# Kernel optimization log

Hardware: AMD Instinct MI355X
Metric: run time of the kernel (lower is better)

## Reference

```python
import jax, jax.numpy as jnp
import numpy as np

N, E, R = 100000, 600000, 2      # nodes, edges per relation, relations
IN, H, DH = 128, 8, 16           # input dim, heads, per-head hidden
D = H * DH                       # 128 = hidden_dim * n_heads
RIN, RH = 64, 16                 # relation input / hidden dims
SLOPE = 0.2                      # leaky relu negative slope


def _leaky(v):
    return jnp.where(v >= 0, v, SLOPE * v)


def setup_inputs() -> dict:
    key = jax.random.key(0)
    ks = jax.random.split(key, 18)
    nrm = lambda k, shape, s: jax.random.normal(k, shape, jnp.float32) * s
    sc = 1.0 / np.sqrt(D).astype(np.float32)
    return {
        'x': nrm(ks[0], (N, IN), 1.0),
        'src': jax.random.randint(ks[1], (R, E), 0, N, jnp.int32),
        'dst': jax.random.randint(ks[2], (R, E), 0, N, jnp.int32),
        'rel_emb': nrm(ks[3], (R, RIN), 1.0),
        'Wp': nrm(ks[4], (IN, D), sc), 'bp': jnp.zeros((D,), jnp.float32),
        'Wn': nrm(ks[5], (D, D), sc), 'bn': jnp.zeros((D,), jnp.float32),
        'Wsrc': nrm(ks[6], (R, D, D), sc), 'bsrc': jnp.zeros((R, D), jnp.float32),
        'Wrel': nrm(ks[7], (R, RIN, H * 2 * DH), 1.0 / np.sqrt(RIN).astype(np.float32)),
        'resW': nrm(ks[8], (IN, D), sc), 'resb': jnp.zeros((D,), jnp.float32),
        'res_alpha': nrm(ks[9], (1,), 1.0),
        'crossW': nrm(ks[10], (R, H, DH), 1.0 / np.sqrt(DH).astype(np.float32)),
        'Wprop': nrm(ks[11], (R, RIN, H * RH), 1.0 / np.sqrt(RIN).astype(np.float32)),
        'bprop': jnp.zeros((R, H * RH), jnp.float32),
    }


def reference(x, src, dst, rel_emb, Wp, bp, Wn, bn, Wsrc, bsrc, Wrel,
              resW, resb, res_alpha, crossW, Wprop, bprop):
    # projection_layer (R_HGT) then node_transformation_layers (layer input transform)
    xp = x @ Wp + bp                                  # [N, D]
    h = (xp @ Wn + bn).reshape(N, H, DH)              # [N, H, DH] dst-side features
    res = (xp @ resW + resb).reshape(N, H, DH)        # res_fc(input_dst)

    def per_rel(sr, dr, e_emb, Ws, bs, Wr):
        # relation_src_node_transformation + relation-conditioned attention
        s = (h.reshape(N, D) @ Ws + bs).reshape(N, H, DH)   # src messages
        a = (e_emb @ Wr).reshape(H, 2, DH)                  # relation attn vectors
        sc_src = (s * a[:, 0]).sum(-1)                      # [N, H]
        sc_dst = (h * a[:, 1]).sum(-1)                      # [N, H]
        e_sc = _leaky(sc_src[sr] + sc_dst[dr])              # [E, H]
        # edge softmax over incoming edges of each dst node
        m = jax.lax.stop_gradient(jax.ops.segment_max(e_sc, dr, num_segments=N))
        ex = jnp.exp(e_sc - m[dr])
        den = jax.ops.segment_sum(ex, dr, num_segments=N)
        alpha = ex / den[dr]                                # [E, H]
        msg = alpha[:, :, None] * s[sr]                     # [E, H, DH]
        return jax.ops.segment_sum(msg, dr, num_segments=N)  # [N, H, DH]

    out = jax.vmap(per_rel)(src, dst, rel_emb, Wsrc, bsrc, Wrel)  # [R, N, H, DH]

    # sigmoid-gated residual (shared per dst ntype)
    g = jax.nn.sigmoid(res_alpha)[0]
    out = out * g + res[None] * (1.0 - g)

    # RelationCrossing: attention across the R relation-specific dst features
    def cross(cw):
        attn = jax.nn.softmax(_leaky((out * cw[None, None]).sum(-1)), axis=0)  # [R,N,H]
        return (attn[..., None] * out).sum(0)                                  # [N,H,DH]

    fused = jax.vmap(cross)(crossW).reshape(R, N, D)      # [R, N, D]

    # relation_propagation_layer
    rel_out = jnp.einsum('ri,rio->ro', rel_emb, Wprop) + bprop  # [R, H*RH]
    return fused, rel_out
```

## Files before the change

kernel.cpp:

```cpp
#include <hip/hip_runtime.h>
#include <math.h>

#define NN 100000
#define EE 600000
#define RR 2
#define DD 128
#define HH 8
#define DHH 16
#define RN (RR * NN)
#define NT 26
#define MTOT 6250
#define CHUNK 4096
#define NCH ((EE + CHUNK - 1) / CHUNK)
#define BINW 512
#define NBIN ((NN + BINW - 1) / BINW)
#define BCAPD 4096

typedef unsigned short ushort_t;
typedef short bf16x8 __attribute__((ext_vector_type(8)));
typedef float f32x4 __attribute__((ext_vector_type(4)));

__device__ __forceinline__ float lrelu(float v) { return v >= 0.f ? v : 0.2f * v; }

__device__ __forceinline__ ushort_t f2bf(float f) {
    unsigned int u = __float_as_uint(f);
    u = (u + 0x7FFFu + ((u >> 16) & 1u)) >> 16;
    return (ushort_t)u;
}
__device__ __forceinline__ float bf2f(ushort_t u) {
    return __uint_as_float(((unsigned int)u) << 16);
}

__global__ void k_prep(const float* __restrict__ rel_emb, const float* __restrict__ Wrel,
                       const float* __restrict__ Wprop, const float* __restrict__ bprop,
                       float* __restrict__ avec, float* __restrict__ rel_out) {
    int tid = threadIdx.x;
    for (int idx = tid; idx < RR * 256; idx += 256) {
        int r = idx >> 8, o = idx & 255;
        float acc = 0.f;
        for (int i = 0; i < 64; ++i)
            acc += rel_emb[r * 64 + i] * Wrel[(r * 64 + i) * 256 + o];
        avec[idx] = acc;
    }
    {
        int r = tid >> 7, o = tid & 127;
        float acc = bprop[tid];
        for (int i = 0; i < 64; ++i)
            acc += rel_emb[r * 64 + i] * Wprop[(r * 64 + i) * 128 + o];
        rel_out[tid] = acc;
    }
}

__global__ __launch_bounds__(128) void k_compose1(
    const float* __restrict__ Wp, const float* __restrict__ bp,
    const float* __restrict__ Wn, const float* __restrict__ bn,
    const float* __restrict__ resW, const float* __restrict__ resb,
    float* __restrict__ Wpn, float* __restrict__ bpn,
    float* __restrict__ Wres_c, float* __restrict__ bres_c) {
    __shared__ float row[DD];
    const int rrow = blockIdx.x, tid = threadIdx.x;
    row[tid] = Wp[rrow * DD + tid];
    __syncthreads();
    float acc1 = 0.f, acc2 = 0.f;
    for (int k = 0; k < DD; ++k) {
        float wv = row[k];
        acc1 = fmaf(wv, Wn[k * DD + tid], acc1);
        acc2 = fmaf(wv, resW[k * DD + tid], acc2);
    }
    Wpn[rrow * DD + tid] = acc1;
    Wres_c[rrow * DD + tid] = acc2;
    if (rrow == 0) {
        float b1 = 0.f, b2 = 0.f;
        for (int k = 0; k < DD; ++k) {
            b1 = fmaf(bp[k], Wn[k * DD + tid], b1);
            b2 = fmaf(bp[k], resW[k * DD + tid], b2);
        }
        bpn[tid] = b1 + bn[tid];
        bres_c[tid] = b2 + resb[tid];
    }
}

__global__ __launch_bounds__(128) void k_compose2(
    const float* __restrict__ Wpn, const float* __restrict__ bpn,
    const float* __restrict__ Wsrc, const float* __restrict__ bsrc,
    const float* __restrict__ avec,
    float* __restrict__ Ws_c, float* __restrict__ bs_c,
    float* __restrict__ VdstT, float* __restrict__ cdst) {
    __shared__ float row[DD];
    const int rel = blockIdx.x, rrow = blockIdx.y, tid = threadIdx.x;
    row[tid] = Wpn[rrow * DD + tid];
    __syncthreads();
    const float* W = Wsrc + (size_t)rel * DD * DD;
    float acc = 0.f;
    for (int k = 0; k < DD; ++k) acc = fmaf(row[k], W[k * DD + tid], acc);
    Ws_c[(size_t)rel * DD * DD + rrow * DD + tid] = acc;
    if (tid < HH) {
        float v = 0.f;
        for (int d = 0; d < 16; ++d)
            v += row[tid * 16 + d] * avec[rel * 256 + tid * 32 + 16 + d];
        VdstT[(rel * HH + tid) * DD + rrow] = v;
    }
    if (rrow == 0) {
        float b = 0.f;
        for (int k = 0; k < DD; ++k) b = fmaf(bpn[k], W[k * DD + tid], b);
        bs_c[rel * DD + tid] = b + bsrc[rel * DD + tid];
        if (rel == 0 && tid < 16) {
            int r2 = tid >> 3, h2 = tid & 7;
            float c2 = 0.f;
            for (int d = 0; d < 16; ++d)
                c2 += bpn[h2 * 16 + d] * avec[r2 * 256 + h2 * 32 + 16 + d];
            cdst[tid] = c2;
        }
    }
}

__global__ __launch_bounds__(256) void k_pack(
    const float* __restrict__ Ws_c, const float* __restrict__ Wres_c,
    const float* __restrict__ VdstT, const float* __restrict__ avec,
    const float* __restrict__ bs_c, short* __restrict__ Wpk,
    float* __restrict__ csrc) {
    const int t = blockIdx.x;
    const int kt = threadIdx.x >> 6;
    const int l = threadIdx.x & 63;
    const int c16 = l & 15;
    bf16x8 v;
    #pragma unroll
    for (int j = 0; j < 8; ++j) {
        int k = kt * 32 + (l >> 4) * 8 + j;
        float f;
        if (t < 24) {
            int m = t >> 3;
            int col = (t & 7) * 16 + c16;
            const float* W = (m == 0) ? Ws_c : (m == 1) ? Ws_c + DD * DD : Wres_c;
            f = W[k * DD + col];
        } else if (t == 24) {
            f = VdstT[c16 * DD + k];
        } else {
            int rel = c16 >> 3, h = c16 & 7;
            f = 0.f;
            for (int d = 0; d < 16; ++d)
                f += Ws_c[(size_t)rel * DD * DD + k * DD + h * 16 + d]
                     * avec[rel * 256 + h * 32 + d];
        }
        v[j] = (short)f2bf(f);
    }
    *(bf16x8*)(Wpk + ((size_t)(t * 4 + kt) * 64 + l) * 8) = v;
    if (t == 25 && threadIdx.x < 16) {
        int rel = threadIdx.x >> 3, h = threadIdx.x & 7;
        float c = 0.f;
        for (int d = 0; d < 16; ++d)
            c += bs_c[rel * DD + h * 16 + d] * avec[rel * 256 + h * 32 + d];
        csrc[threadIdx.x] = c;
    }
}

__global__ __launch_bounds__(256) void k_node3(
    const float* __restrict__ x, const short* __restrict__ Wpk,
    const float* __restrict__ bs_c, const float* __restrict__ bres_c,
    const float* __restrict__ cdst, const float* __restrict__ csrc,
    ushort_t* __restrict__ s_out, ushort_t* __restrict__ res_out,
    float* __restrict__ sc_src, float* __restrict__ sc_dst) {
    const int tid = threadIdx.x;
    const int l = tid & 63;
    const int w = tid >> 6;
    const int m16 = l & 15, g4 = l >> 4;
    const int mt = blockIdx.x * 4 + w;
    const bool live = (mt < MTOT);
    const int nb = (live ? mt : MTOT - 1) * 16;

    bf16x8 af[4];
    const float* xrow = x + (size_t)(nb + m16) * DD + g4 * 8;
    #pragma unroll
    for (int kt = 0; kt < 4; ++kt) {
        float4 v0 = *(const float4*)(xrow + kt * 32);
        float4 v1 = *(const float4*)(xrow + kt * 32 + 4);
        af[kt][0] = (short)f2bf(v0.x); af[kt][1] = (short)f2bf(v0.y);
        af[kt][2] = (short)f2bf(v0.z); af[kt][3] = (short)f2bf(v0.w);
        af[kt][4] = (short)f2bf(v1.x); af[kt][5] = (short)f2bf(v1.y);
        af[kt][6] = (short)f2bf(v1.z); af[kt][7] = (short)f2bf(v1.w);
    }

    for (int t = 0; t < NT; ++t) {
        f32x4 acc = {0.f, 0.f, 0.f, 0.f};
        #pragma unroll
        for (int kt = 0; kt < 4; ++kt) {
            bf16x8 b = *(const bf16x8*)(Wpk + ((size_t)(t * 4 + kt) * 64 + l) * 8);
            acc = __builtin_amdgcn_mfma_f32_16x16x32_bf16(af[kt], b, acc, 0, 0, 0);
        }
        if (!live) continue;
        if (t < 16) {
            const int rel = t >> 3, head = t & 7;
            const float bb = bs_c[rel * DD + head * 16 + m16];
            #pragma unroll
            for (int r = 0; r < 4; ++r) {
                const int node = nb + g4 * 4 + r;
                s_out[((size_t)rel * NN + node) * DD + head * 16 + m16] =
                    f2bf(acc[r] + bb);
            }
        } else if (t < 24) {
            const int col = (t - 16) * 16 + m16;
            const float bb = bres_c[col];
            #pragma unroll
            for (int r = 0; r < 4; ++r) {
                const int node = nb + g4 * 4 + r;
                res_out[(size_t)node * DD + col] = f2bf(acc[r] + bb);
            }
        } else if (t == 24) {
            const int rel = m16 >> 3, head = m16 & 7;
            const float bb = cdst[m16];
            #pragma unroll
            for (int r = 0; r < 4; ++r) {
                const int node = nb + g4 * 4 + r;
                sc_dst[((size_t)rel * NN + node) * HH + head] = acc[r] + bb;
            }
        } else {
            const int rel = m16 >> 3, head = m16 & 7;
            const float bb = csrc[m16];
            #pragma unroll
            for (int r = 0; r < 4; ++r) {
                const int node = nb + g4 * 4 + r;
                sc_src[((size_t)rel * NN + node) * HH + head] = acc[r] + bb;
            }
        }
    }
}

__global__ __launch_bounds__(256) void k_binct(const int* __restrict__ dst,
                                               int* __restrict__ binct) {
    __shared__ int bins[NBIN];
    const int blk = blockIdx.x, rel = blockIdx.y, tid = threadIdx.x;
    if (tid < NBIN) bins[tid] = 0;
    __syncthreads();
    for (int i = tid; i < CHUNK; i += 256) {
        int e = blk * CHUNK + i;
        if (e < EE) atomicAdd(&bins[dst[rel * EE + e] >> 9], 1);
    }
    __syncthreads();
    if (tid < NBIN) binct[((rel * NCH) + blk) * NBIN + tid] = bins[tid];
}

__global__ __launch_bounds__(512) void k_binscan(const int* __restrict__ binct,
                                                 int* __restrict__ runoff,
                                                 int* __restrict__ binstart,
                                                 int* __restrict__ row_ptr) {
    __shared__ int tot[512];
    const int t = threadIdx.x;
    int run = 0;
    if (t < RR * NBIN) {
        const int rel = t / NBIN, bin = t - rel * NBIN;
        for (int blk = 0; blk < NCH; ++blk) {
            int idx = ((rel * NCH) + blk) * NBIN + bin;
            int v = binct[idx];
            runoff[idx] = run;
            run += v;
        }
    }
    tot[t] = (t < RR * NBIN) ? run : 0;
    __syncthreads();
    for (int off = 1; off < 512; off <<= 1) {
        int v = (t >= off) ? tot[t - off] : 0;
        __syncthreads();
        tot[t] += v;
        __syncthreads();
    }
    if (t < RR * NBIN) binstart[t] = tot[t] - run;
    if (t == 0) {
        binstart[RR * NBIN] = RR * EE;
        row_ptr[RN] = RR * EE;
    }
}

__global__ __launch_bounds__(256) void k_binfill(
    const int* __restrict__ src, const int* __restrict__ dst,
    const int* __restrict__ runoff, const int* __restrict__ binstart,
    int* __restrict__ ebuf) {
    __shared__ int ofs[NBIN];
    __shared__ int bins[NBIN];
    const int blk = blockIdx.x, rel = blockIdx.y, tid = threadIdx.x;
    if (tid < NBIN) {
        ofs[tid] = binstart[rel * NBIN + tid] + runoff[((rel * NCH) + blk) * NBIN + tid];
        bins[tid] = 0;
    }
    __syncthreads();
    for (int i = tid; i < CHUNK; i += 256) {
        int e = blk * CHUNK + i;
        if (e < EE) {
            int d = dst[rel * EE + e];
            int b = d >> 9;
            int loc = atomicAdd(&bins[b], 1);
            ebuf[ofs[b] + loc] = ((d & 511) << 17) | src[rel * EE + e];
        }
    }
}

__global__ __launch_bounds__(256) void k_binfin(
    const int* __restrict__ ebuf, const int* __restrict__ binstart,
    int* __restrict__ row_ptr, int* __restrict__ esrc) {
    __shared__ int keys[BCAPD];
    __shared__ int cnt[BINW];
    __shared__ int scn[BINW];
    __shared__ int part[256];
    const int bin = blockIdx.x, rel = blockIdx.y, tid = threadIdx.x;
    const int p0 = binstart[rel * NBIN + bin];
    const int p1 = binstart[rel * NBIN + bin + 1];
    const int cntE = p1 - p0;
    const bool inlds = (cntE <= BCAPD);
    const int n0 = bin * BINW;
    const int nw = min(BINW, NN - n0);

    cnt[2 * tid] = 0; cnt[2 * tid + 1] = 0;
    __syncthreads();
    for (int i = tid; i < cntE; i += 256) {
        int k = ebuf[p0 + i];
        if (inlds) keys[i] = k;
        atomicAdd(&cnt[k >> 17], 1);
    }
    __syncthreads();
    int a = cnt[2 * tid], b = cnt[2 * tid + 1];
    part[tid] = a + b;
    __syncthreads();
    for (int off = 1; off < 256; off <<= 1) {
        int v = (tid >= off) ? part[tid - off] : 0;
        __syncthreads();
        part[tid] += v;
        __syncthreads();
    }
    int excl = (tid == 0) ? 0 : part[tid - 1];
    scn[2 * tid] = excl;
    scn[2 * tid + 1] = excl + a;
    cnt[2 * tid] = 0; cnt[2 * tid + 1] = 0;
    __syncthreads();
    for (int n = tid; n < nw; n += 256)
        row_ptr[rel * NN + n0 + n] = p0 + scn[n];
    for (int i = tid; i < cntE; i += 256) {
        int k = inlds ? keys[i] : ebuf[p0 + i];
        int low = k >> 17;
        int slot = atomicAdd(&cnt[low], 1);
        esrc[p0 + scn[low] + slot] = k & 0x1FFFF;
    }
}

__global__ __launch_bounds__(256) void k_gather_cross(
    const int* __restrict__ esrc, const int* __restrict__ row_ptr,
    const float* __restrict__ sc_src, const float* __restrict__ sc_dst,
    const ushort_t* __restrict__ s, const ushort_t* __restrict__ res_buf,
    const float* __restrict__ res_alpha, const float* __restrict__ crossW,
    float* __restrict__ out) {
    int n = blockIdx.x * 4 + (threadIdx.x >> 6);
    if (n >= NN) return;
    const int lane = threadIdx.x & 63;
    const int g = lane >> 5;
    const int j = lane & 31;
    const int h = j >> 2;

    const int seg = g * NN + n;
    const int p0 = row_ptr[seg], p1 = row_ptr[seg + 1];
    const float sd = sc_dst[(size_t)seg * HH + h];

    float den = 0.f;
    float4 acc = {0.f, 0.f, 0.f, 0.f};
    int p = p0;
    for (; p + 1 < p1; p += 2) {
        int sr0 = esrc[p], sr1 = esrc[p + 1];
        ushort4 s40 = *(const ushort4*)(s + (size_t)(g * NN + sr0) * DD + j * 4);
        ushort4 s41 = *(const ushort4*)(s + (size_t)(g * NN + sr1) * DD + j * 4);
        float v0 = lrelu(sc_src[(size_t)(g * NN + sr0) * HH + h] + sd);
        float v1 = lrelu(sc_src[(size_t)(g * NN + sr1) * HH + h] + sd);
        float e0 = __expf(v0);
        float e1 = __expf(v1);
        den += e0; den += e1;
        acc.x = fmaf(e0, bf2f(s40.x), acc.x); acc.x = fmaf(e1, bf2f(s41.x), acc.x);
        acc.y = fmaf(e0, bf2f(s40.y), acc.y); acc.y = fmaf(e1, bf2f(s41.y), acc.y);
        acc.z = fmaf(e0, bf2f(s40.z), acc.z); acc.z = fmaf(e1, bf2f(s41.z), acc.z);
        acc.w = fmaf(e0, bf2f(s40.w), acc.w); acc.w = fmaf(e1, bf2f(s41.w), acc.w);
    }
    if (p < p1) {
        int sr0 = esrc[p];
        ushort4 s40 = *(const ushort4*)(s + (size_t)(g * NN + sr0) * DD + j * 4);
        float v0 = lrelu(sc_src[(size_t)(g * NN + sr0) * HH + h] + sd);
        float e0 = __expf(v0);
        den += e0;
        acc.x = fmaf(e0, bf2f(s40.x), acc.x);
        acc.y = fmaf(e0, bf2f(s40.y), acc.y);
        acc.z = fmaf(e0, bf2f(s40.z), acc.z);
        acc.w = fmaf(e0, bf2f(s40.w), acc.w);
    }
    float inv = (p1 > p0) ? 1.f / den : 0.f;

    float gate = 1.f / (1.f + __expf(-res_alpha[0]));
    ushort4 r4u = *(const ushort4*)(res_buf + (size_t)n * DD + j * 4);
    float4 og;
    og.x = fmaf(acc.x * inv, gate, bf2f(r4u.x) * (1.f - gate));
    og.y = fmaf(acc.y * inv, gate, bf2f(r4u.y) * (1.f - gate));
    og.z = fmaf(acc.z * inv, gate, bf2f(r4u.z) * (1.f - gate));
    og.w = fmaf(acc.w * inv, gate, bf2f(r4u.w) * (1.f - gate));

    float4 oo;
    oo.x = __shfl_xor(og.x, 32);
    oo.y = __shfl_xor(og.y, 32);
    oo.z = __shfl_xor(og.z, 32);
    oo.w = __shfl_xor(og.w, 32);

    float4 cw = *(const float4*)(crossW + g * DD + j * 4);
    float ds_ = og.x * cw.x + og.y * cw.y + og.z * cw.z + og.w * cw.w;
    float do_ = oo.x * cw.x + oo.y * cw.y + oo.z * cw.z + oo.w * cw.w;
    ds_ += __shfl_xor(ds_, 1); ds_ += __shfl_xor(ds_, 2);
    do_ += __shfl_xor(do_, 1); do_ += __shfl_xor(do_, 2);
    float l0 = lrelu(ds_), l1 = lrelu(do_);
    float mm = fmaxf(l0, l1);
    float e0 = __expf(l0 - mm), e1 = __expf(l1 - mm);
    float winv = 1.f / (e0 + e1);
    float w0 = e0 * winv, w1 = e1 * winv;

    float4 o;
    o.x = w0 * og.x + w1 * oo.x;
    o.y = w0 * og.y + w1 * oo.y;
    o.z = w0 * og.z + w1 * oo.z;
    o.w = w0 * og.w + w1 * oo.w;
    *(float4*)(out + (size_t)(g * NN + n) * DD + j * 4) = o;
}

extern "C" void kernel_launch(void* const* d_in, const int* in_sizes, int n_in,
                              void* d_out, int out_size, void* d_ws, size_t ws_size,
                              hipStream_t stream) {
    const float* x        = (const float*)d_in[0];
    const int*   src      = (const int*)d_in[1];
    const int*   dst      = (const int*)d_in[2];
    const float* rel_emb  = (const float*)d_in[3];
    const float* Wp       = (const float*)d_in[4];
    const float* bp       = (const float*)d_in[5];
    const float* Wn       = (const float*)d_in[6];
    const float* bn       = (const float*)d_in[7];
    const float* Wsrc     = (const float*)d_in[8];
    const float* bsrc     = (const float*)d_in[9];
    const float* Wrel     = (const float*)d_in[10];
    const float* resW     = (const float*)d_in[11];
    const float* resb     = (const float*)d_in[12];
    const float* res_alpha= (const float*)d_in[13];
    const float* crossW   = (const float*)d_in[14];
    const float* Wprop    = (const float*)d_in[15];
    const float* bprop    = (const float*)d_in[16];

    float* out = (float*)d_out;

    ushort_t* s_bf   = (ushort_t*)d_ws;
    ushort_t* res_bf = s_bf + (size_t)RR * NN * DD;
    float* fbase   = (float*)(res_bf + (size_t)NN * DD);
    float* sc_src  = fbase;
    float* sc_dst  = sc_src  + (size_t)RR * NN * HH;
    float* avec    = sc_dst  + (size_t)RR * NN * HH;
    float* Wpn     = avec    + 512;
    float* Wres_c  = Wpn     + DD * DD;
    float* Ws_c    = Wres_c  + DD * DD;
    float* VdstT   = Ws_c    + (size_t)RR * DD * DD;
    float* bpn     = VdstT   + 16 * DD;
    float* bres_c  = bpn     + DD;
    float* bs_c    = bres_c  + DD;
    float* cdst    = bs_c    + RR * DD;
    float* csrc    = cdst    + 16;
    short* Wpk     = (short*)(csrc + 16);
    int*   row_ptr = (int*)(Wpk + (size_t)NT * 4 * 64 * 8);
    int*   binct   = row_ptr + RN + 1;
    int*   runoff  = binct + RR * NCH * NBIN;
    int*   binstart= runoff + RR * NCH * NBIN;
    int*   ebuf    = binstart + RR * NBIN + 1;
    int*   esrc    = ebuf + RR * EE;

    k_prep<<<1, 256, 0, stream>>>(rel_emb, Wrel, Wprop, bprop, avec,
                                  out + (size_t)RR * NN * DD);
    k_compose1<<<DD, DD, 0, stream>>>(Wp, bp, Wn, bn, resW, resb,
                                      Wpn, bpn, Wres_c, bres_c);
    k_compose2<<<dim3(RR, DD), DD, 0, stream>>>(Wpn, bpn, Wsrc, bsrc, avec,
                                                Ws_c, bs_c, VdstT, cdst);
    k_pack<<<NT, 256, 0, stream>>>(Ws_c, Wres_c, VdstT, avec, bs_c, Wpk, csrc);
    k_node3<<<(MTOT + 3) / 4, 256, 0, stream>>>(
        x, Wpk, bs_c, bres_c, cdst, csrc, s_bf, res_bf, sc_src, sc_dst);
    k_binct<<<dim3(NCH, RR), 256, 0, stream>>>(dst, binct);
    k_binscan<<<1, 512, 0, stream>>>(binct, runoff, binstart, row_ptr);
    k_binfill<<<dim3(NCH, RR), 256, 0, stream>>>(src, dst, runoff, binstart, ebuf);
    k_binfin<<<dim3(NBIN, RR), 256, 0, stream>>>(ebuf, binstart, row_ptr, esrc);
    k_gather_cross<<<(NN + 3) / 4, 256, 0, stream>>>(esrc, row_ptr, sc_src, sc_dst,
                                                     s_bf, res_bf, res_alpha, crossW,
                                                     out);
}
```

Measured before the change: 228.1 us.

## Merge prep and bin-count kernels into neighbors, add nontemporal accesses, split accumulators

Folds the small k_prep kernel into k_compose1 using spare blocks, and runs the bin-count stage as extra blocks appended to the node GEMM kernel, which removes two launches and lets independent work overlap. Streaming loads and stores in binfill, binfin and gather_cross are marked nontemporal to reduce cache pollution. The gather loop now keeps two independent accumulator sets to shorten the FMA dependency chains. The trade-offs are a slightly different summation order and heterogeneous blocks within k_node3.

```diff
diff --git a/kernel.cpp b/kernel.cpp
--- a/kernel.cpp
+++ b/kernel.cpp
@@ -10,6 +10,7 @@
 #define RN (RR * NN)
 #define NT 26
 #define MTOT 6250
+#define NB3 ((MTOT + 3) / 4)
 #define CHUNK 4096
 #define NCH ((EE + CHUNK - 1) / CHUNK)
 #define BINW 512
@@ -19,6 +20,7 @@
 typedef unsigned short ushort_t;
 typedef short bf16x8 __attribute__((ext_vector_type(8)));
 typedef float f32x4 __attribute__((ext_vector_type(4)));
+typedef unsigned short u16x4 __attribute__((ext_vector_type(4)));
 
 __device__ __forceinline__ float lrelu(float v) { return v >= 0.f ? v : 0.2f * v; }
 
@@ -31,32 +33,15 @@
     return __uint_as_float(((unsigned int)u) << 16);
 }
 
-__global__ void k_prep(const float* __restrict__ rel_emb, const float* __restrict__ Wrel,
-                       const float* __restrict__ Wprop, const float* __restrict__ bprop,
-                       float* __restrict__ avec, float* __restrict__ rel_out) {
-    int tid = threadIdx.x;
-    for (int idx = tid; idx < RR * 256; idx += 256) {
-        int r = idx >> 8, o = idx & 255;
-        float acc = 0.f;
-        for (int i = 0; i < 64; ++i)
-            acc += rel_emb[r * 64 + i] * Wrel[(r * 64 + i) * 256 + o];
-        avec[idx] = acc;
-    }
-    {
-        int r = tid >> 7, o = tid & 127;
-        float acc = bprop[tid];
-        for (int i = 0; i < 64; ++i)
-            acc += rel_emb[r * 64 + i] * Wprop[(r * 64 + i) * 128 + o];
-        rel_out[tid] = acc;
-    }
-}
-
 __global__ __launch_bounds__(128) void k_compose1(
     const float* __restrict__ Wp, const float* __restrict__ bp,
     const float* __restrict__ Wn, const float* __restrict__ bn,
     const float* __restrict__ resW, const float* __restrict__ resb,
+    const float* __restrict__ rel_emb, const float* __restrict__ Wrel,
+    const float* __restrict__ Wprop, const float* __restrict__ bprop,
     float* __restrict__ Wpn, float* __restrict__ bpn,
-    float* __restrict__ Wres_c, float* __restrict__ bres_c) {
+    float* __restrict__ Wres_c, float* __restrict__ bres_c,
+    float* __restrict__ avec, float* __restrict__ rel_out) {
     __shared__ float row[DD];
     const int rrow = blockIdx.x, tid = threadIdx.x;
     row[tid] = Wp[rrow * DD + tid];
@@ -77,6 +62,21 @@
         }
         bpn[tid] = b1 + bn[tid];
         bres_c[tid] = b2 + resb[tid];
+    }
+    if (rrow < 4) {
+        int idx = rrow * DD + tid;
+        int r = idx >> 8, o = idx & 255;
+        float acc = 0.f;
+        for (int i = 0; i < 64; ++i)
+            acc += rel_emb[r * 64 + i] * Wrel[(r * 64 + i) * 256 + o];
+        avec[idx] = acc;
+    } else if (rrow < 6) {
+        int o = (rrow - 4) * DD + tid;
+        int r = o >> 7, oo = o & 127;
+        float acc = bprop[o];
+        for (int i = 0; i < 64; ++i)
+            acc += rel_emb[r * 64 + i] * Wprop[(r * 64 + i) * 128 + oo];
+        rel_out[o] = acc;
     }
 }
 
@@ -158,8 +158,25 @@
     const float* __restrict__ x, const short* __restrict__ Wpk,
     const float* __restrict__ bs_c, const float* __restrict__ bres_c,
     const float* __restrict__ cdst, const float* __restrict__ csrc,
+    const int* __restrict__ dst, int* __restrict__ binct,
     ushort_t* __restrict__ s_out, ushort_t* __restrict__ res_out,
     float* __restrict__ sc_src, float* __restrict__ sc_dst) {
+    if (blockIdx.x >= NB3) {
+        __shared__ int bins[NBIN];
+        const int b = blockIdx.x - NB3;
+        const int rel = b / NCH, blk = b - rel * NCH;
+        const int tid = threadIdx.x;
+        if (tid < NBIN) bins[tid] = 0;
+        __syncthreads();
+        for (int i = tid; i < CHUNK; i += 256) {
+            int e = blk * CHUNK + i;
+            if (e < EE)
+                atomicAdd(&bins[__builtin_nontemporal_load(dst + rel * EE + e) >> 9], 1);
+        }
+        __syncthreads();
+        if (tid < NBIN) binct[((rel * NCH) + blk) * NBIN + tid] = bins[tid];
+        return;
+    }
     const int tid = threadIdx.x;
     const int l = tid & 63;
     const int w = tid >> 6;
@@ -225,20 +242,6 @@
     }
 }
 
-__global__ __launch_bounds__(256) void k_binct(const int* __restrict__ dst,
-                                               int* __restrict__ binct) {
-    __shared__ int bins[NBIN];
-    const int blk = blockIdx.x, rel = blockIdx.y, tid = threadIdx.x;
-    if (tid < NBIN) bins[tid] = 0;
-    __syncthreads();
-    for (int i = tid; i < CHUNK; i += 256) {
-        int e = blk * CHUNK + i;
-        if (e < EE) atomicAdd(&bins[dst[rel * EE + e] >> 9], 1);
-    }
-    __syncthreads();
-    if (tid < NBIN) binct[((rel * NCH) + blk) * NBIN + tid] = bins[tid];
-}
-
 __global__ __launch_bounds__(512) void k_binscan(const int* __restrict__ binct,
                                                  int* __restrict__ runoff,
                                                  int* __restrict__ binstart,
@@ -285,10 +288,11 @@
     for (int i = tid; i < CHUNK; i += 256) {
         int e = blk * CHUNK + i;
         if (e < EE) {
-            int d = dst[rel * EE + e];
+            int d = __builtin_nontemporal_load(dst + rel * EE + e);
             int b = d >> 9;
             int loc = atomicAdd(&bins[b], 1);
-            ebuf[ofs[b] + loc] = ((d & 511) << 17) | src[rel * EE + e];
+            ebuf[ofs[b] + loc] =
+                ((d & 511) << 17) | __builtin_nontemporal_load(src + rel * EE + e);
         }
     }
 }
@@ -311,7 +315,7 @@
     cnt[2 * tid] = 0; cnt[2 * tid + 1] = 0;
     __syncthreads();
     for (int i = tid; i < cntE; i += 256) {
-        int k = ebuf[p0 + i];
+        int k = __builtin_nontemporal_load(ebuf + p0 + i);
         if (inlds) keys[i] = k;
         atomicAdd(&cnt[k >> 17], 1);
     }
@@ -357,8 +361,8 @@
     const int p0 = row_ptr[seg], p1 = row_ptr[seg + 1];
     const float sd = sc_dst[(size_t)seg * HH + h];
 
-    float den = 0.f;
-    float4 acc = {0.f, 0.f, 0.f, 0.f};
+    float den0 = 0.f, den1 = 0.f;
+    float4 acc0 = {0.f, 0.f, 0.f, 0.f}, acc1 = {0.f, 0.f, 0.f, 0.f};
     int p = p0;
     for (; p + 1 < p1; p += 2) {
         int sr0 = esrc[p], sr1 = esrc[p + 1];
@@ -368,32 +372,35 @@
         float v1 = lrelu(sc_src[(size_t)(g * NN + sr1) * HH + h] + sd);
         float e0 = __expf(v0);
         float e1 = __expf(v1);
-        den += e0; den += e1;
-        acc.x = fmaf(e0, bf2f(s40.x), acc.x); acc.x = fmaf(e1, bf2f(s41.x), acc.x);
-        acc.y = fmaf(e0, bf2f(s40.y), acc.y); acc.y = fmaf(e1, bf2f(s41.y), acc.y);
-        acc.z = fmaf(e0, bf2f(s40.z), acc.z); acc.z = fmaf(e1, bf2f(s41.z), acc.z);
-        acc.w = fmaf(e0, bf2f(s40.w), acc.w); acc.w = fmaf(e1, bf2f(s41.w), acc.w);
+        den0 += e0; den1 += e1;
+        acc0.x = fmaf(e0, bf2f(s40.x), acc0.x); acc1.x = fmaf(e1, bf2f(s41.x), acc1.x);
+        acc0.y = fmaf(e0, bf2f(s40.y), acc0.y); acc1.y = fmaf(e1, bf2f(s41.y), acc1.y);
+        acc0.z = fmaf(e0, bf2f(s40.z), acc0.z); acc1.z = fmaf(e1, bf2f(s41.z), acc1.z);
+        acc0.w = fmaf(e0, bf2f(s40.w), acc0.w); acc1.w = fmaf(e1, bf2f(s41.w), acc1.w);
     }
     if (p < p1) {
         int sr0 = esrc[p];
         ushort4 s40 = *(const ushort4*)(s + (size_t)(g * NN + sr0) * DD + j * 4);
         float v0 = lrelu(sc_src[(size_t)(g * NN + sr0) * HH + h] + sd);
         float e0 = __expf(v0);
-        den += e0;
-        acc.x = fmaf(e0, bf2f(s40.x), acc.x);
-        acc.y = fmaf(e0, bf2f(s40.y), acc.y);
-        acc.z = fmaf(e0, bf2f(s40.z), acc.z);
-        acc.w = fmaf(e0, bf2f(s40.w), acc.w);
-    }
+        den0 += e0;
+        acc0.x = fmaf(e0, bf2f(s40.x), acc0.x);
+        acc0.y = fmaf(e0, bf2f(s40.y), acc0.y);
+        acc0.z = fmaf(e0, bf2f(s40.z), acc0.z);
+        acc0.w = fmaf(e0, bf2f(s40.w), acc0.w);
+    }
+    float den = den0 + den1;
+    float4 acc = {acc0.x + acc1.x, acc0.y + acc1.y, acc0.z + acc1.z, acc0.w + acc1.w};
     float inv = (p1 > p0) ? 1.f / den : 0.f;
 
     float gate = 1.f / (1.f + __expf(-res_alpha[0]));
-    ushort4 r4u = *(const ushort4*)(res_buf + (size_t)n * DD + j * 4);
+    u16x4 r4u = __builtin_nontemporal_load(
+        (const u16x4*)(res_buf + (size_t)n * DD + j * 4));
     float4 og;
-    og.x = fmaf(acc.x * inv, gate, bf2f(r4u.x) * (1.f - gate));
-    og.y = fmaf(acc.y * inv, gate, bf2f(r4u.y) * (1.f - gate));
-    og.z = fmaf(acc.z * inv, gate, bf2f(r4u.z) * (1.f - gate));
-    og.w = fmaf(acc.w * inv, gate, bf2f(r4u.w) * (1.f - gate));
+    og.x = fmaf(acc.x * inv, gate, bf2f(r4u[0]) * (1.f - gate));
+    og.y = fmaf(acc.y * inv, gate, bf2f(r4u[1]) * (1.f - gate));
+    og.z = fmaf(acc.z * inv, gate, bf2f(r4u[2]) * (1.f - gate));
+    og.w = fmaf(acc.w * inv, gate, bf2f(r4u[3]) * (1.f - gate));
 
     float4 oo;
     oo.x = __shfl_xor(og.x, 32);
@@ -412,12 +419,12 @@
     float winv = 1.f / (e0 + e1);
     float w0 = e0 * winv, w1 = e1 * winv;
 
-    float4 o;
-    o.x = w0 * og.x + w1 * oo.x;
-    o.y = w0 * og.y + w1 * oo.y;
-    o.z = w0 * og.z + w1 * oo.z;
-    o.w = w0 * og.w + w1 * oo.w;
-    *(float4*)(out + (size_t)(g * NN + n) * DD + j * 4) = o;
+    f32x4 o;
+    o[0] = w0 * og.x + w1 * oo.x;
+    o[1] = w0 * og.y + w1 * oo.y;
+    o[2] = w0 * og.z + w1 * oo.z;
+    o[3] = w0 * og.w + w1 * oo.w;
+    __builtin_nontemporal_store(o, (f32x4*)(out + (size_t)(g * NN + n) * DD + j * 4));
 }
 
 extern "C" void kernel_launch(void* const* d_in, const int* in_sizes, int n_in,
@@ -466,16 +473,16 @@
     int*   ebuf    = binstart + RR * NBIN + 1;
     int*   esrc    = ebuf + RR * EE;
 
-    k_prep<<<1, 256, 0, stream>>>(rel_emb, Wrel, Wprop, bprop, avec,
-                                  out + (size_t)RR * NN * DD);
     k_compose1<<<DD, DD, 0, stream>>>(Wp, bp, Wn, bn, resW, resb,
-                                      Wpn, bpn, Wres_c, bres_c);
+                                      rel_emb, Wrel, Wprop, bprop,
+                                      Wpn, bpn, Wres_c, bres_c,
+                                      avec, out + (size_t)RR * NN * DD);
     k_compose2<<<dim3(RR, DD), DD, 0, stream>>>(Wpn, bpn, Wsrc, bsrc, avec,
                                                 Ws_c, bs_c, VdstT, cdst);
     k_pack<<<NT, 256, 0, stream>>>(Ws_c, Wres_c, VdstT, avec, bs_c, Wpk, csrc);
-    k_node3<<<(MTOT + 3) / 4, 256, 0, stream>>>(
-        x, Wpk, bs_c, bres_c, cdst, csrc, s_bf, res_bf, sc_src, sc_dst);
-    k_binct<<<dim3(NCH, RR), 256, 0, stream>>>(dst, binct);
+    k_node3<<<NB3 + RR * NCH, 256, 0, stream>>>(
+        x, Wpk, bs_c, bres_c, cdst, csrc, dst, binct,
+        s_bf, res_bf, sc_src, sc_dst);
     k_binscan<<<1, 512, 0, stream>>>(binct, runoff, binstart, row_ptr);
     k_binfill<<<dim3(NCH, RR), 256, 0, stream>>>(src, dst, runoff, binstart, ebuf);
     k_binfin<<<dim3(NBIN, RR), 256, 0, stream>>>(ebuf, binstart, row_ptr, esrc);
```

Result: faster. 209.3 us (-8.3%).
